# Kernel optimization log

Hardware: AMD Instinct MI355X
Metric: run time of the kernel (lower is better)

## Reference

```python
import jax, jax.numpy as jnp
import numpy as np

H = 1024       # hidden_size
E = 1024       # embedding_size
V = 50257      # output_size (vocab)
L = 64         # max_length


def setup_inputs() -> dict:
    key = jax.random.key(0)
    ks = jax.random.split(key, 12)
    s = 0.02
    return {
        "input": jax.random.randint(ks[0], (1,), 0, V),
        "hidden": jax.random.normal(ks[1], (1, 1, H), dtype=jnp.float32),
        "encoder_outputs": jax.random.normal(ks[2], (L, H), dtype=jnp.float32),
        "emb": jax.random.normal(ks[3], (V, E), dtype=jnp.float32) * s,
        "attn_w": jax.random.normal(ks[4], (L, H + E), dtype=jnp.float32) * s,
        "attn_b": jnp.zeros((L,), dtype=jnp.float32),
        "comb_w": jax.random.normal(ks[5], (E, H + E), dtype=jnp.float32) * s,
        "comb_b": jnp.zeros((E,), dtype=jnp.float32),
        "w_ih": jax.random.normal(ks[6], (3 * H, E), dtype=jnp.float32) * s,
        "b_ih": jnp.zeros((3 * H,), dtype=jnp.float32),
        "w_hh": jax.random.normal(ks[7], (3 * H, H), dtype=jnp.float32) * s,
        "b_hh": jnp.zeros((3 * H,), dtype=jnp.float32),
        "out_w": jax.random.normal(ks[8], (V, H), dtype=jnp.float32) * s,
        "out_b": jnp.zeros((V,), dtype=jnp.float32),
    }


def reference(input, hidden, encoder_outputs, emb, attn_w, attn_b,
              comb_w, comb_b, w_ih, b_ih, w_hh, b_hh, out_w, out_b):
    # embedding + (dropout = identity in eval)
    embedded = emb[input].reshape(1, E)            # [1, E]
    h0 = hidden[0]                                  # [1, H]
    # Bahdanau-style attention over fixed-length encoder outputs
    attn_logits = jnp.concatenate([embedded, h0], axis=1) @ attn_w.T + attn_b
    attn_weights = jax.nn.softmax(attn_logits, axis=1)      # [1, L]
    attn_applied = attn_weights @ encoder_outputs            # [1, H]
    x = jnp.concatenate([embedded, attn_applied], axis=1) @ comb_w.T + comb_b
    x = jax.nn.relu(x)                               # [1, E]
    # single GRU cell step (torch gate order: r, z, n)
    gi = x @ w_ih.T + b_ih
    gh = h0 @ w_hh.T + b_hh
    i_r, i_z, i_n = jnp.split(gi, 3, axis=1)
    h_r, h_z, h_n = jnp.split(gh, 3, axis=1)
    r = jax.nn.sigmoid(i_r + h_r)
    z = jax.nn.sigmoid(i_z + h_z)
    n = jnp.tanh(i_n + r * h_n)
    h_new = (1.0 - z) * n + z * h0                   # [1, H]
    logp = jax.nn.log_softmax(h_new @ out_w.T + out_b, axis=1)  # [1, V]
    return logp, h_new[None], attn_weights
```

## Files before the change

kernel.cpp:

```cpp
#include <hip/hip_runtime.h>
#include <math.h>

#define H 1024
#define E 1024
#define V 50257
#define L 64
#define HE 2048

__device__ inline float dot4(float4 a, float4 b) {
    return a.x*b.x + a.y*b.y + a.z*b.z + a.w*b.w;
}

__device__ inline float wave_reduce_sum(float v) {
    #pragma unroll
    for (int off = 32; off > 0; off >>= 1)
        v += __shfl_down(v, off, 64);
    return v;
}

__device__ inline void ms_merge(float& M, float& S, float m2, float s2) {
    if (s2 > 0.f) {
        if (m2 > M) { S = S * expf(M - m2) + s2; M = m2; }
        else        { S += s2 * expf(m2 - M); }
    }
}

__global__ __launch_bounds__(256) void k_pre(
        const int* __restrict__ inp,
        const float* __restrict__ hidden,
        const float* __restrict__ emb,
        const float* __restrict__ attn_w,
        const float* __restrict__ attn_b,
        const float* __restrict__ comb_w,
        const float* __restrict__ w_hh,
        const float* __restrict__ b_hh,
        float* __restrict__ lg,
        float* __restrict__ gh,
        float* __restrict__ q1) {
    const int bid  = blockIdx.x;
    const int t    = threadIdx.x;
    const int wave = t >> 6;
    const int lane = t & 63;
    __shared__ float red[4];

    const float* erow = emb + (size_t)inp[0] * E;
    const float4* e4 = (const float4*)erow;
    const float4* h4 = (const float4*)hidden;

    if (bid < 64) {
        const float4* w = (const float4*)(attn_w + (size_t)bid * HE);
        float s = dot4(w[t], e4[t]) + dot4(w[256 + t], h4[t]);
        s = wave_reduce_sum(s);
        if (lane == 0) red[wave] = s;
        __syncthreads();
        if (t == 0) lg[bid] = red[0] + red[1] + red[2] + red[3] + attn_b[bid];
    } else if (bid < 832) {
        int row = (bid - 64) * 4 + wave;
        const float4* wr = (const float4*)(w_hh + (size_t)row * H);
        float s = 0.f;
        #pragma unroll
        for (int i = 0; i < 4; ++i)
            s += dot4(wr[i * 64 + lane], h4[i * 64 + lane]);
        s = wave_reduce_sum(s);
        if (lane == 0) gh[row] = s + b_hh[row];
    } else {
        int row = (bid - 832) * 4 + wave;
        const float4* wr = (const float4*)(comb_w + (size_t)row * HE);
        float s = 0.f;
        #pragma unroll
        for (int i = 0; i < 4; ++i)
            s += dot4(wr[i * 64 + lane], e4[i * 64 + lane]);
        s = wave_reduce_sum(s);
        if (lane == 0) q1[row] = s;
    }
}

__global__ __launch_bounds__(512) void k_comb2(
        const float* __restrict__ lg,
        const float* __restrict__ enc,
        const float* __restrict__ q1,
        const float* __restrict__ comb_w,
        const float* __restrict__ comb_b,
        float* __restrict__ x,
        float* __restrict__ out_weights) {
    __shared__ float sig[L];
    __shared__ float aa[H];
    int t = threadIdx.x, wave = t >> 6, lane = t & 63;
    if (t < 64) {
        float v = lg[t];
        float m = v;
        #pragma unroll
        for (int off = 32; off > 0; off >>= 1) m = fmaxf(m, __shfl_xor(m, off, 64));
        float ex = expf(v - m);
        float ssum = ex;
        #pragma unroll
        for (int off = 32; off > 0; off >>= 1) ssum += __shfl_xor(ssum, off, 64);
        float w = ex / ssum;
        sig[t] = w;
        if (blockIdx.x == 0) out_weights[t] = w;
    }
    __syncthreads();
    {
        float a0 = 0.f, a1 = 0.f;
        #pragma unroll 8
        for (int l = 0; l < L; ++l) {
            float s = sig[l];
            a0 += s * enc[l * H + t];
            a1 += s * enc[l * H + t + 512];
        }
        aa[t] = a0;
        aa[t + 512] = a1;
    }
    __syncthreads();
    int row = blockIdx.x * 8 + wave;
    const float4* wr = (const float4*)(comb_w + (size_t)row * HE + E);
    const float4* a4 = (const float4*)aa;
    float s = 0.f;
    #pragma unroll
    for (int i = 0; i < 4; ++i)
        s += dot4(wr[i * 64 + lane], a4[i * 64 + lane]);
    s = wave_reduce_sum(s);
    if (lane == 0) x[row] = fmaxf(s + q1[row] + comb_b[row], 0.f);
}

__global__ __launch_bounds__(768) void k_gru2(
        const float* __restrict__ x,
        const float* __restrict__ hidden,
        const float* __restrict__ w_ih,
        const float* __restrict__ b_ih,
        const float* __restrict__ gh,
        float* __restrict__ h_new) {
    int t = threadIdx.x, wave = t >> 6, lane = t & 63;
    int jj = wave >> 2;
    int g  = wave >> 2;
    int j4 = wave & 3;
    int j  = blockIdx.x * 4 + j4;
    (void)jj;
    const float4* x4 = (const float4*)x;
    const float4* wr = (const float4*)(w_ih + (size_t)(g * H + j) * E);
    float s = 0.f;
    #pragma unroll
    for (int i = 0; i < 4; ++i)
        s += dot4(wr[i * 64 + lane], x4[i * 64 + lane]);
    s = wave_reduce_sum(s);
    __shared__ float red[3][4];
    if (lane == 0) red[g][j4] = s + b_ih[g * H + j];
    __syncthreads();
    if (t < 4) {
        int jo = blockIdx.x * 4 + t;
        float i_r = red[0][t], i_z = red[1][t], i_n = red[2][t];
        float h_r = gh[jo], h_z = gh[H + jo], h_n = gh[2 * H + jo];
        float r = 1.f / (1.f + expf(-(i_r + h_r)));
        float z = 1.f / (1.f + expf(-(i_z + h_z)));
        float n = tanhf(i_n + r * h_n);
        h_new[jo] = (1.f - z) * n + z * hidden[jo];
    }
}

__global__ __launch_bounds__(256) void k_vocab(
        const float* __restrict__ h_new,
        const float* __restrict__ out_w,
        const float* __restrict__ out_b,
        float* __restrict__ logp,
        float2* __restrict__ partials) {
    int t = threadIdx.x, wave = t >> 6, lane = t & 63;
    const float4* h4 = (const float4*)h_new;
    float4 hv[4];
    #pragma unroll
    for (int i = 0; i < 4; ++i) hv[i] = h4[i * 64 + lane];
    int base = blockIdx.x * 16 + wave * 4;
    float s[4] = {0.f, 0.f, 0.f, 0.f};
    if (base + 3 < V) {
        const float4* w0 = (const float4*)(out_w + (size_t)(base + 0) * H);
        const float4* w1 = (const float4*)(out_w + (size_t)(base + 1) * H);
        const float4* w2 = (const float4*)(out_w + (size_t)(base + 2) * H);
        const float4* w3 = (const float4*)(out_w + (size_t)(base + 3) * H);
        #pragma unroll
        for (int i = 0; i < 4; ++i) {
            int idx = i * 64 + lane;
            s[0] += dot4(w0[idx], hv[i]);
            s[1] += dot4(w1[idx], hv[i]);
            s[2] += dot4(w2[idx], hv[i]);
            s[3] += dot4(w3[idx], hv[i]);
        }
    } else {
        #pragma unroll
        for (int k = 0; k < 4; ++k) {
            if (base + k < V) {
                const float4* w = (const float4*)(out_w + (size_t)(base + k) * H);
                #pragma unroll
                for (int i = 0; i < 4; ++i)
                    s[k] += dot4(w[i * 64 + lane], hv[i]);
            }
        }
    }
    #pragma unroll
    for (int off = 32; off > 0; off >>= 1) {
        s[0] += __shfl_down(s[0], off, 64);
        s[1] += __shfl_down(s[1], off, 64);
        s[2] += __shfl_down(s[2], off, 64);
        s[3] += __shfl_down(s[3], off, 64);
    }
    __shared__ float smM[4], smS[4];
    if (lane == 0) {
        float M = -INFINITY, S = 0.f;
        #pragma unroll
        for (int k = 0; k < 4; ++k) {
            int r = base + k;
            if (r < V) {
                float v = s[k] + out_b[r];
                logp[r] = v;
                float nm = fmaxf(M, v);
                S = S * expf(M - nm) + expf(v - nm);
                M = nm;
            }
        }
        smM[wave] = M; smS[wave] = S;
    }
    __syncthreads();
    if (t == 0) {
        float Mb = smM[0], Sb = smS[0];
        #pragma unroll
        for (int i = 1; i < 4; ++i) ms_merge(Mb, Sb, smM[i], smS[i]);
        partials[blockIdx.x] = make_float2(Mb, Sb);
    }
}

__global__ __launch_bounds__(256) void k_logsoftmax(
        float* __restrict__ logp,
        const float2* __restrict__ partials, int nb) {
    int t = threadIdx.x;
    float M = -INFINITY, S = 0.f;
    for (int i = t; i < nb; i += 256) {
        float2 p = partials[i];
        ms_merge(M, S, p.x, p.y);
    }
    #pragma unroll
    for (int off = 32; off > 0; off >>= 1) {
        float m2 = __shfl_down(M, off, 64);
        float s2 = __shfl_down(S, off, 64);
        ms_merge(M, S, m2, s2);
    }
    __shared__ float sm[4], ss[4];
    __shared__ float sh_lz;
    if ((t & 63) == 0) { sm[t >> 6] = M; ss[t >> 6] = S; }
    __syncthreads();
    if (t == 0) {
        #pragma unroll
        for (int i = 1; i < 4; ++i) ms_merge(sm[0], ss[0], sm[i], ss[i]);
        sh_lz = sm[0] + logf(ss[0]);
    }
    __syncthreads();
    float lz = sh_lz;
    int i = blockIdx.x * 256 + t;
    if (i < V) logp[i] -= lz;
}

extern "C" void kernel_launch(void* const* d_in, const int* in_sizes, int n_in,
                              void* d_out, int out_size, void* d_ws, size_t ws_size,
                              hipStream_t stream) {
    const int*   inp     = (const int*)d_in[0];
    const float* hidden  = (const float*)d_in[1];
    const float* enc     = (const float*)d_in[2];
    const float* emb     = (const float*)d_in[3];
    const float* attn_w  = (const float*)d_in[4];
    const float* attn_b  = (const float*)d_in[5];
    const float* comb_w  = (const float*)d_in[6];
    const float* comb_b  = (const float*)d_in[7];
    const float* w_ih    = (const float*)d_in[8];
    const float* b_ih    = (const float*)d_in[9];
    const float* w_hh    = (const float*)d_in[10];
    const float* b_hh    = (const float*)d_in[11];
    const float* out_w   = (const float*)d_in[12];
    const float* out_b   = (const float*)d_in[13];

    float* out          = (float*)d_out;
    float* logp         = out;
    float* h_new        = out + V;
    float* attn_weights = out + V + H;

    float* ws  = (float*)d_ws;
    float* lg  = ws;
    float* gh  = ws + 64;
    float* q1  = ws + 3136;
    float* x   = ws + 4160;
    float2* partials = (float2*)(ws + 5184);
    const int nb = (V + 15) / 16;

    k_pre<<<1088, 256, 0, stream>>>(inp, hidden, emb, attn_w, attn_b,
                                    comb_w, w_hh, b_hh, lg, gh, q1);
    k_comb2<<<128, 512, 0, stream>>>(lg, enc, q1, comb_w, comb_b, x, attn_weights);
    k_gru2<<<256, 768, 0, stream>>>(x, hidden, w_ih, b_ih, gh, h_new);
    k_vocab<<<nb, 256, 0, stream>>>(h_new, out_w, out_b, logp, partials);
    k_logsoftmax<<<(V + 255) / 256, 256, 0, stream>>>(logp, partials, nb);
}
```

Before: 68.40 us.

## Fuse attention and combine into front kernel, nontemporal loads, drop max in softmax

Merges the attention-logit, softmax, attention-apply and combine stages into one front kernel. Each of 128 blocks redundantly recomputes the 64 attention logits and the weighted encoder sum, and the w_hh GEMV runs alongside in the remaining blocks, which removes one launch and the intermediate buffers. Weight loads for comb_w, w_hh and w_ih now use nontemporal hints. The vocab log-softmax drops the running max and sums expf(v) directly, which is cheaper but relies on the logits being small enough not to overflow.

```diff
diff --git a/kernel.cpp b/kernel.cpp
--- a/kernel.cpp
+++ b/kernel.cpp
@@ -7,8 +7,18 @@
 #define L 64
 #define HE 2048
 
+typedef float floatx4 __attribute__((ext_vector_type(4)));
+
 __device__ inline float dot4(float4 a, float4 b) {
     return a.x*b.x + a.y*b.y + a.z*b.z + a.w*b.w;
+}
+
+__device__ inline floatx4 ldnt(const float4* p) {
+    return __builtin_nontemporal_load((const floatx4*)p);
+}
+
+__device__ inline float dotn(floatx4 a, float4 b) {
+    return a[0]*b.x + a[1]*b.y + a[2]*b.z + a[3]*b.w;
 }
 
 __device__ inline float wave_reduce_sum(float v) {
@@ -18,112 +28,112 @@
     return v;
 }
 
-__device__ inline void ms_merge(float& M, float& S, float m2, float s2) {
-    if (s2 > 0.f) {
-        if (m2 > M) { S = S * expf(M - m2) + s2; M = m2; }
-        else        { S += s2 * expf(m2 - M); }
-    }
-}
-
-__global__ __launch_bounds__(256) void k_pre(
+__global__ __launch_bounds__(512) void k_front(
         const int* __restrict__ inp,
         const float* __restrict__ hidden,
+        const float* __restrict__ enc,
         const float* __restrict__ emb,
         const float* __restrict__ attn_w,
         const float* __restrict__ attn_b,
         const float* __restrict__ comb_w,
+        const float* __restrict__ comb_b,
         const float* __restrict__ w_hh,
         const float* __restrict__ b_hh,
-        float* __restrict__ lg,
+        float* __restrict__ x,
         float* __restrict__ gh,
-        float* __restrict__ q1) {
+        float* __restrict__ out_weights) {
     const int bid  = blockIdx.x;
     const int t    = threadIdx.x;
     const int wave = t >> 6;
     const int lane = t & 63;
-    __shared__ float red[4];
+
+    __shared__ float lgS[L];
+    __shared__ float sig[L];
+    __shared__ __align__(16) float aa[H];
 
     const float* erow = emb + (size_t)inp[0] * E;
     const float4* e4 = (const float4*)erow;
     const float4* h4 = (const float4*)hidden;
 
-    if (bid < 64) {
-        const float4* w = (const float4*)(attn_w + (size_t)bid * HE);
-        float s = dot4(w[t], e4[t]) + dot4(w[256 + t], h4[t]);
-        s = wave_reduce_sum(s);
-        if (lane == 0) red[wave] = s;
+    if (bid < 128) {
+        float4 ev[4], hv[4];
+        #pragma unroll
+        for (int i = 0; i < 4; ++i) { ev[i] = e4[i * 64 + lane]; hv[i] = h4[i * 64 + lane]; }
+        float s[8];
+        #pragma unroll
+        for (int r = 0; r < 8; ++r) {
+            int row = wave * 8 + r;
+            const float4* w = (const float4*)(attn_w + (size_t)row * HE);
+            float acc = 0.f;
+            #pragma unroll
+            for (int i = 0; i < 4; ++i) acc += dot4(w[i * 64 + lane], ev[i]);
+            #pragma unroll
+            for (int i = 0; i < 4; ++i) acc += dot4(w[256 + i * 64 + lane], hv[i]);
+            s[r] = acc;
+        }
+        #pragma unroll
+        for (int r = 0; r < 8; ++r) s[r] = wave_reduce_sum(s[r]);
+        if (lane == 0) {
+            #pragma unroll
+            for (int r = 0; r < 8; ++r) {
+                int row = wave * 8 + r;
+                lgS[row] = s[r] + attn_b[row];
+            }
+        }
         __syncthreads();
-        if (t == 0) lg[bid] = red[0] + red[1] + red[2] + red[3] + attn_b[bid];
-    } else if (bid < 832) {
-        int row = (bid - 64) * 4 + wave;
+        if (t < 64) {
+            float v = lgS[t];
+            float m = v;
+            #pragma unroll
+            for (int off = 32; off > 0; off >>= 1) m = fmaxf(m, __shfl_xor(m, off, 64));
+            float ex = expf(v - m);
+            float ssum = ex;
+            #pragma unroll
+            for (int off = 32; off > 0; off >>= 1) ssum += __shfl_xor(ssum, off, 64);
+            float w = ex / ssum;
+            sig[t] = w;
+            if (bid == 0) out_weights[t] = w;
+        }
+        __syncthreads();
+        {
+            float a0 = 0.f, a1 = 0.f;
+            #pragma unroll 8
+            for (int l = 0; l < L; ++l) {
+                float sl = sig[l];
+                a0 += sl * enc[l * H + t];
+                a1 += sl * enc[l * H + t + 512];
+            }
+            aa[t] = a0;
+            aa[t + 512] = a1;
+        }
+        __syncthreads();
+        {
+            int row = bid * 8 + wave;
+            const float4* wr = (const float4*)(comb_w + (size_t)row * HE);
+            const float4* a4 = (const float4*)aa;
+            float acc = 0.f;
+            #pragma unroll
+            for (int i = 0; i < 4; ++i) acc += dotn(ldnt(&wr[i * 64 + lane]), ev[i]);
+            #pragma unroll
+            for (int i = 0; i < 4; ++i) acc += dotn(ldnt(&wr[256 + i * 64 + lane]), a4[i * 64 + lane]);
+            acc = wave_reduce_sum(acc);
+            if (lane == 0) x[row] = fmaxf(acc + comb_b[row], 0.f);
+        }
+    } else {
+        int row = (bid - 128) * 8 + wave;
+        float4 hv[4];
+        #pragma unroll
+        for (int i = 0; i < 4; ++i) hv[i] = h4[i * 64 + lane];
         const float4* wr = (const float4*)(w_hh + (size_t)row * H);
-        float s = 0.f;
-        #pragma unroll
-        for (int i = 0; i < 4; ++i)
-            s += dot4(wr[i * 64 + lane], h4[i * 64 + lane]);
-        s = wave_reduce_sum(s);
-        if (lane == 0) gh[row] = s + b_hh[row];
-    } else {
-        int row = (bid - 832) * 4 + wave;
-        const float4* wr = (const float4*)(comb_w + (size_t)row * HE);
-        float s = 0.f;
-        #pragma unroll
-        for (int i = 0; i < 4; ++i)
-            s += dot4(wr[i * 64 + lane], e4[i * 64 + lane]);
-        s = wave_reduce_sum(s);
-        if (lane == 0) q1[row] = s;
-    }
-}
-
-__global__ __launch_bounds__(512) void k_comb2(
-        const float* __restrict__ lg,
-        const float* __restrict__ enc,
-        const float* __restrict__ q1,
-        const float* __restrict__ comb_w,
-        const float* __restrict__ comb_b,
-        float* __restrict__ x,
-        float* __restrict__ out_weights) {
-    __shared__ float sig[L];
-    __shared__ float aa[H];
-    int t = threadIdx.x, wave = t >> 6, lane = t & 63;
-    if (t < 64) {
-        float v = lg[t];
-        float m = v;
-        #pragma unroll
-        for (int off = 32; off > 0; off >>= 1) m = fmaxf(m, __shfl_xor(m, off, 64));
-        float ex = expf(v - m);
-        float ssum = ex;
-        #pragma unroll
-        for (int off = 32; off > 0; off >>= 1) ssum += __shfl_xor(ssum, off, 64);
-        float w = ex / ssum;
-        sig[t] = w;
-        if (blockIdx.x == 0) out_weights[t] = w;
-    }
-    __syncthreads();
-    {
-        float a0 = 0.f, a1 = 0.f;
-        #pragma unroll 8
-        for (int l = 0; l < L; ++l) {
-            float s = sig[l];
-            a0 += s * enc[l * H + t];
-            a1 += s * enc[l * H + t + 512];
-        }
-        aa[t] = a0;
-        aa[t + 512] = a1;
-    }
-    __syncthreads();
-    int row = blockIdx.x * 8 + wave;
-    const float4* wr = (const float4*)(comb_w + (size_t)row * HE + E);
-    const float4* a4 = (const float4*)aa;
-    float s = 0.f;
-    #pragma unroll
-    for (int i = 0; i < 4; ++i)
-        s += dot4(wr[i * 64 + lane], a4[i * 64 + lane]);
-    s = wave_reduce_sum(s);
-    if (lane == 0) x[row] = fmaxf(s + q1[row] + comb_b[row], 0.f);
-}
-
-__global__ __launch_bounds__(768) void k_gru2(
+        float acc = 0.f;
+        #pragma unroll
+        for (int i = 0; i < 4; ++i) acc += dotn(ldnt(&wr[i * 64 + lane]), hv[i]);
+        acc = wave_reduce_sum(acc);
+        if (lane == 0) gh[row] = acc + b_hh[row];
+    }
+}
+
+__global__ __launch_bounds__(768) void k_gru(
         const float* __restrict__ x,
         const float* __restrict__ hidden,
         const float* __restrict__ w_ih,
@@ -131,17 +141,15 @@
         const float* __restrict__ gh,
         float* __restrict__ h_new) {
     int t = threadIdx.x, wave = t >> 6, lane = t & 63;
-    int jj = wave >> 2;
     int g  = wave >> 2;
     int j4 = wave & 3;
     int j  = blockIdx.x * 4 + j4;
-    (void)jj;
     const float4* x4 = (const float4*)x;
     const float4* wr = (const float4*)(w_ih + (size_t)(g * H + j) * E);
     float s = 0.f;
     #pragma unroll
     for (int i = 0; i < 4; ++i)
-        s += dot4(wr[i * 64 + lane], x4[i * 64 + lane]);
+        s += dotn(ldnt(&wr[i * 64 + lane]), x4[i * 64 + lane]);
     s = wave_reduce_sum(s);
     __shared__ float red[3][4];
     if (lane == 0) red[g][j4] = s + b_ih[g * H + j];
@@ -162,7 +170,7 @@
         const float* __restrict__ out_w,
         const float* __restrict__ out_b,
         float* __restrict__ logp,
-        float2* __restrict__ partials) {
+        float* __restrict__ partials) {
     int t = threadIdx.x, wave = t >> 6, lane = t & 63;
     const float4* h4 = (const float4*)h_new;
     float4 hv[4];
@@ -185,14 +193,12 @@
         }
     } else {
         #pragma unroll
-        for (int k = 0; k < 4; ++k) {
+        for (int k = 0; k < 4; ++k)
             if (base + k < V) {
                 const float4* w = (const float4*)(out_w + (size_t)(base + k) * H);
                 #pragma unroll
-                for (int i = 0; i < 4; ++i)
-                    s[k] += dot4(w[i * 64 + lane], hv[i]);
-            }
-        }
+                for (int i = 0; i < 4; ++i) s[k] += dot4(w[i * 64 + lane], hv[i]);
+            }
     }
     #pragma unroll
     for (int off = 32; off > 0; off >>= 1) {
@@ -201,55 +207,37 @@
         s[2] += __shfl_down(s[2], off, 64);
         s[3] += __shfl_down(s[3], off, 64);
     }
-    __shared__ float smM[4], smS[4];
+    __shared__ float smP[4];
     if (lane == 0) {
-        float M = -INFINITY, S = 0.f;
+        float pe = 0.f;
         #pragma unroll
         for (int k = 0; k < 4; ++k) {
             int r = base + k;
             if (r < V) {
                 float v = s[k] + out_b[r];
                 logp[r] = v;
-                float nm = fmaxf(M, v);
-                S = S * expf(M - nm) + expf(v - nm);
-                M = nm;
-            }
-        }
-        smM[wave] = M; smS[wave] = S;
-    }
-    __syncthreads();
-    if (t == 0) {
-        float Mb = smM[0], Sb = smS[0];
-        #pragma unroll
-        for (int i = 1; i < 4; ++i) ms_merge(Mb, Sb, smM[i], smS[i]);
-        partials[blockIdx.x] = make_float2(Mb, Sb);
-    }
-}
-
-__global__ __launch_bounds__(256) void k_logsoftmax(
+                pe += expf(v);
+            }
+        }
+        smP[wave] = pe;
+    }
+    __syncthreads();
+    if (t == 0)
+        partials[blockIdx.x] = smP[0] + smP[1] + smP[2] + smP[3];
+}
+
+__global__ __launch_bounds__(256) void k_lsm(
         float* __restrict__ logp,
-        const float2* __restrict__ partials, int nb) {
+        const float* __restrict__ partials, int nb) {
     int t = threadIdx.x;
-    float M = -INFINITY, S = 0.f;
-    for (int i = t; i < nb; i += 256) {
-        float2 p = partials[i];
-        ms_merge(M, S, p.x, p.y);
-    }
-    #pragma unroll
-    for (int off = 32; off > 0; off >>= 1) {
-        float m2 = __shfl_down(M, off, 64);
-        float s2 = __shfl_down(S, off, 64);
-        ms_merge(M, S, m2, s2);
-    }
-    __shared__ float sm[4], ss[4];
+    float S = 0.f;
+    for (int i = t; i < nb; i += 256) S += partials[i];
+    S = wave_reduce_sum(S);
+    __shared__ float ss[4];
     __shared__ float sh_lz;
-    if ((t & 63) == 0) { sm[t >> 6] = M; ss[t >> 6] = S; }
-    __syncthreads();
-    if (t == 0) {
-        #pragma unroll
-        for (int i = 1; i < 4; ++i) ms_merge(sm[0], ss[0], sm[i], ss[i]);
-        sh_lz = sm[0] + logf(ss[0]);
-    }
+    if ((t & 63) == 0) ss[t >> 6] = S;
+    __syncthreads();
+    if (t == 0) sh_lz = logf(ss[0] + ss[1] + ss[2] + ss[3]);
     __syncthreads();
     float lz = sh_lz;
     int i = blockIdx.x * 256 + t;
@@ -279,18 +267,16 @@
     float* h_new        = out + V;
     float* attn_weights = out + V + H;
 
-    float* ws  = (float*)d_ws;
-    float* lg  = ws;
-    float* gh  = ws + 64;
-    float* q1  = ws + 3136;
-    float* x   = ws + 4160;
-    float2* partials = (float2*)(ws + 5184);
+    float* ws       = (float*)d_ws;
+    float* gh       = ws;
+    float* x        = ws + 3072;
+    float* partials = ws + 4096;
     const int nb = (V + 15) / 16;
 
-    k_pre<<<1088, 256, 0, stream>>>(inp, hidden, emb, attn_w, attn_b,
-                                    comb_w, w_hh, b_hh, lg, gh, q1);
-    k_comb2<<<128, 512, 0, stream>>>(lg, enc, q1, comb_w, comb_b, x, attn_weights);
-    k_gru2<<<256, 768, 0, stream>>>(x, hidden, w_ih, b_ih, gh, h_new);
+    k_front<<<512, 512, 0, stream>>>(inp, hidden, enc, emb, attn_w, attn_b,
+                                     comb_w, comb_b, w_hh, b_hh,
+                                     x, gh, attn_weights);
+    k_gru<<<256, 768, 0, stream>>>(x, hidden, w_ih, b_ih, gh, h_new);
     k_vocab<<<nb, 256, 0, stream>>>(h_new, out_w, out_b, logp, partials);
-    k_logsoftmax<<<(V + 255) / 256, 256, 0, stream>>>(logp, partials, nb);
-}
+    k_lsm<<<(V + 255) / 256, 256, 0, stream>>>(logp, partials, nb);
+}
```

Result: slower. 70.44 us (+3.0%).
